# Optimization experiments

Measured on AMD Instinct MI355X. Metric: run time of the kernel, lower is better.

## Reference

```python
import jax, jax.numpy as jnp
import numpy as np

NQ = 4  # circuit is hard-wired to a 4-qubit ring
INV_SQRT2 = 1.0 / float(np.sqrt(2.0))


def _apply_1q(state, g, w):
    # state: [E,2,2,2,2]; g: [2,2] (shared) or [E,2,2] (per-edge)
    state = jnp.moveaxis(state, 1 + w, -1)
    sub = 'eab,e...b->e...a' if g.ndim == 3 else 'ab,e...b->e...a'
    state = jnp.einsum(sub, g, state)
    return jnp.moveaxis(state, -1, 1 + w)


def _apply_cry(state, theta, c, t):
    # controlled-RY(theta) with control wire c, target wire t; theta: [E]
    st = jnp.moveaxis(state, (1 + c, 1 + t), (-2, -1))  # [..., c, t]
    co = jnp.cos(theta / 2)[:, None, None]
    si = jnp.sin(theta / 2)[:, None, None]
    a = st[..., 1, 0]
    b = st[..., 1, 1]
    n0 = co * a - si * b
    n1 = si * a + co * b
    st = jnp.stack([jnp.stack([st[..., 0, 0], st[..., 0, 1]], axis=-1),
                    jnp.stack([n0, n1], axis=-1)], axis=-2)
    return jnp.moveaxis(st, (-2, -1), (1 + c, 1 + t))


def _simulate(q, k, params):
    # q, k: [E, NQ] rotation angles; params: [NQ, 3]
    E = q.shape[0]
    state = jnp.zeros((E, 2 ** NQ), jnp.complex64).at[:, 0].set(1.0)
    state = state.reshape((E,) + (2,) * NQ)
    # RY(query[i]) on wire i
    for w in range(NQ):
        c = jnp.cos(q[:, w] / 2)
        s = jnp.sin(q[:, w] / 2)
        g = jnp.stack([jnp.stack([c, -s], -1), jnp.stack([s, c], -1)], -2)
        state = _apply_1q(state, g.astype(jnp.complex64), w)
    # Hadamard on all wires
    H = jnp.array([[1, 1], [1, -1]], jnp.complex64) * INV_SQRT2
    for w in range(NQ):
        state = _apply_1q(state, H, w)
    # CRY(key[i]) on (i, (i+1)%NQ)
    for w in range(NQ):
        state = _apply_cry(state, k[:, w], w, (w + 1) % NQ)
    # Rot(phi, theta, omega) = RZ(omega) RY(theta) RZ(phi) on each wire
    for w in range(NQ):
        phi, th, om = params[w, 0], params[w, 1], params[w, 2]
        ct = jnp.cos(th / 2)
        st_ = jnp.sin(th / 2)
        g = jnp.stack([
            jnp.stack([jnp.exp(-1j * (phi + om) / 2) * ct, -jnp.exp(1j * (phi - om) / 2) * st_]),
            jnp.stack([jnp.exp(-1j * (phi - om) / 2) * st_, jnp.exp(1j * (phi + om) / 2) * ct]),
        ]).astype(jnp.complex64)
        state = _apply_1q(state, g, w)
    # <Z_i> expectation values
    p = jnp.abs(state) ** 2  # [E,2,2,2,2] float32
    exps = []
    for i in range(NQ):
        axes = tuple(a for a in range(1, 1 + NQ) if a != 1 + i)
        m = p.sum(axes)  # [E, 2]
        exps.append(m[:, 0] - m[:, 1])
    return jnp.stack(exps, -1).mean(-1)  # [E]


def setup_inputs() -> dict:
    key = jax.random.key(0)
    ks = jax.random.split(key, 7)
    N, D, E = 50000, 256, 800000
    node_features = jax.random.normal(ks[0], (N, D), jnp.float32)
    edge_index = jax.random.randint(ks[1], (2, E), 0, N)
    Wq = jax.random.normal(ks[2], (NQ, D), jnp.float32) / np.float32(np.sqrt(D))
    bq = jnp.zeros((NQ,), jnp.float32)
    Wk = jax.random.normal(ks[3], (NQ, D), jnp.float32) / np.float32(np.sqrt(D))
    bk = jnp.zeros((NQ,), jnp.float32)
    quantum_params = jax.random.normal(ks[4], (NQ, 3), jnp.float32) * 0.1
    return {'node_features': node_features, 'edge_index': edge_index,
            'Wq': Wq, 'bq': bq, 'Wk': Wk, 'bk': bk,
            'quantum_params': quantum_params}


def reference(node_features, edge_index, Wq, bq, Wk, bk, quantum_params):
    half_pi = np.float32(np.pi / 2)
    queries = jnp.tanh(node_features @ Wq.T + bq) * half_pi  # [N, NQ]
    keys = jnp.tanh(node_features @ Wk.T + bk) * half_pi     # [N, NQ]
    qe = queries[edge_index[0]]  # [E, NQ]
    ke = keys[edge_index[1]]     # [E, NQ]
    attn = _simulate(qe, ke, quantum_params)  # [E]
    return jax.nn.softmax(attn, axis=0)
```

## Files before the change

### kernel.cpp

```cpp
#include <hip/hip_runtime.h>
#include <math.h>

#define HALF_PI   1.57079632679489662f
#define INV_SQRT2 0.70710678118654752f
#define NPART     1024

__global__ __launch_bounds__(256) void node_qk(
        const float* __restrict__ feat,
        const float* __restrict__ Wq, const float* __restrict__ bq,
        const float* __restrict__ Wk, const float* __restrict__ bk,
        float* __restrict__ qtab, float* __restrict__ ktab, int N) {
    const int lane  = threadIdx.x & 63;
    const int wid   = (int)((blockIdx.x * blockDim.x + threadIdx.x) >> 6);
    const int nwid  = (int)((gridDim.x * blockDim.x) >> 6);

    float4 wq4[4], wk4[4];
    #pragma unroll
    for (int q = 0; q < 4; ++q) {
        wq4[q] = reinterpret_cast<const float4*>(Wq + q * 256)[lane];
        wk4[q] = reinterpret_cast<const float4*>(Wk + q * 256)[lane];
    }
    const int  g    = lane >> 3;
    const float bias = (g < 4) ? bq[g] : bk[g & 3];
    const bool hi  = (lane & 32) != 0;
    const bool s16 = (lane & 16) != 0;
    const bool s8  = (lane & 8)  != 0;

    for (int nb = wid * 2; nb < N; nb += nwid * 2) {
        const int  n1ok = (nb + 1 < N);
        float4 f0 = reinterpret_cast<const float4*>(feat)[(size_t)nb * 64 + lane];
        float4 f1 = n1ok ? reinterpret_cast<const float4*>(feat)[(size_t)(nb + 1) * 64 + lane]
                         : make_float4(0.f, 0.f, 0.f, 0.f);

        float acc0[8], acc1[8];
        #pragma unroll
        for (int q = 0; q < 4; ++q) {
            acc0[q]     = f0.x * wq4[q].x + f0.y * wq4[q].y + f0.z * wq4[q].z + f0.w * wq4[q].w;
            acc0[4 + q] = f0.x * wk4[q].x + f0.y * wk4[q].y + f0.z * wk4[q].z + f0.w * wk4[q].w;
            acc1[q]     = f1.x * wq4[q].x + f1.y * wq4[q].y + f1.z * wq4[q].z + f1.w * wq4[q].w;
            acc1[4 + q] = f1.x * wk4[q].x + f1.y * wk4[q].y + f1.z * wk4[q].z + f1.w * wk4[q].w;
        }

        #pragma unroll
        for (int p = 0; p < 2; ++p) {
            float* acc = (p == 0) ? acc0 : acc1;
            #pragma unroll
            for (int j = 0; j < 4; ++j) {
                float give = hi ? acc[j] : acc[j + 4];
                float r = __shfl_xor(give, 32, 64);
                acc[j]     += hi ? 0.f : r;
                acc[j + 4] += hi ? r : 0.f;
            }
            #pragma unroll
            for (int j = 0; j < 2; ++j) {
                float giveLow  = hi ? acc[6 + j] : acc[2 + j];
                float giveHigh = hi ? acc[4 + j] : acc[j];
                float give = s16 ? giveHigh : giveLow;
                float r = __shfl_xor(give, 16, 64);
                acc[j]     += (!hi && !s16) ? r : 0.f;
                acc[2 + j] += (!hi &&  s16) ? r : 0.f;
                acc[4 + j] += ( hi && !s16) ? r : 0.f;
                acc[6 + j] += ( hi &&  s16) ? r : 0.f;
            }
            float a_even = hi ? (s16 ? acc[6] : acc[4]) : (s16 ? acc[2] : acc[0]);
            float a_odd  = hi ? (s16 ? acc[7] : acc[5]) : (s16 ? acc[3] : acc[1]);
            float give3 = s8 ? a_even : a_odd;
            float r3 = __shfl_xor(give3, 8, 64);
            float v = (s8 ? a_odd : a_even) + r3;
            v += __shfl_xor(v, 4, 64);
            v += __shfl_xor(v, 2, 64);
            v += __shfl_xor(v, 1, 64);

            const int n = nb + p;
            if ((p == 0 || n1ok) && (lane & 7) == 0) {
                float t = tanhf(v + bias) * HALF_PI;
                if (g < 4) qtab[(size_t)n * 4 + g] = t;
                else       ktab[(size_t)n * 4 + (g & 3)] = t;
            }
        }
    }
}

__device__ __forceinline__ float edge_ex(float4 qv, float4 kv,
                                         const float* scz, const float* scx) {
    float qa[4] = {qv.x, qv.y, qv.z, qv.w};
    float ka[4] = {kv.x, kv.y, kv.z, kv.w};
    float u[4][2];
    #pragma unroll
    for (int w = 0; w < 4; ++w) {
        float s, c;
        __sincosf(qa[w] * 0.5f, &s, &c);
        u[w][0] = (c + s) * INV_SQRT2;
        u[w][1] = (c - s) * INV_SQRT2;
    }
    float a[16];
    #pragma unroll
    for (int x = 0; x < 16; ++x)
        a[x] = u[0][(x >> 3) & 1] * u[1][(x >> 2) & 1] *
               u[2][(x >> 1) & 1] * u[3][x & 1];
    #pragma unroll
    for (int w = 0; w < 4; ++w) {
        float si, co;
        __sincosf(ka[w] * 0.5f, &si, &co);
        const int cb = 1 << (3 - w);
        const int tb = 1 << (3 - ((w + 1) & 3));
        #pragma unroll
        for (int x = 0; x < 16; ++x) {
            if ((x & cb) && !(x & tb)) {
                float a0 = a[x], a1 = a[x | tb];
                a[x]      = co * a0 - si * a1;
                a[x | tb] = si * a0 + co * a1;
            }
        }
    }
    float attn = 0.f;
    #pragma unroll
    for (int q = 0; q < 4; ++q) {
        const int bit = 1 << (3 - q);
        float sz = 0.f, sx = 0.f;
        #pragma unroll
        for (int x = 0; x < 16; ++x) {
            float pp = a[x] * a[x];
            sz += (x & bit) ? -pp : pp;
            if (!(x & bit)) sx += a[x] * a[x | bit];
        }
        attn += scz[q] * sz - scx[q] * (2.f * sx);
    }
    return __expf(attn * 0.25f);
}

__global__ __launch_bounds__(256) void edge_attn(
        const int* __restrict__ ei,
        const float4* __restrict__ qtab, const float4* __restrict__ ktab,
        const float* __restrict__ qp,
        float* __restrict__ out, float* __restrict__ partial, int E) {
    __shared__ float scz[4], scx[4];
    __shared__ float red[256];
    const int tid = threadIdx.x;
    if (tid < 4) {
        float phi = qp[3 * tid + 0];
        float th  = qp[3 * tid + 1];
        float sth, cth;
        sincosf(th, &sth, &cth);
        scz[tid] = cth;
        scx[tid] = sth * cosf(phi);
    }
    __syncthreads();

    const int gtid  = blockIdx.x * 256 + tid;
    const int total = NPART * 256;

    int sidx[4], didx[4];
    #pragma unroll
    for (int it = 0; it < 4; ++it) {
        const int e  = gtid + it * total;
        const int ee = (e < E) ? e : (E - 1);
        sidx[it] = ei[ee];
        didx[it] = ei[E + ee];
    }

    float lsum = 0.f;
    #pragma unroll
    for (int it = 0; it < 4; ++it) {
        const int e = gtid + it * total;
        if (e < E) {
            float v = edge_ex(qtab[sidx[it]], ktab[didx[it]], scz, scx);
            out[e] = v;
            lsum += v;
        }
    }

    red[tid] = lsum;
    __syncthreads();
    #pragma unroll
    for (int s = 128; s > 0; s >>= 1) {
        if (tid < s) red[tid] += red[tid + s];
        __syncthreads();
    }
    if (tid == 0) partial[blockIdx.x] = red[0];
}

__global__ __launch_bounds__(256) void normalize_out(
        float* __restrict__ out, const float* __restrict__ partial, int E) {
    __shared__ float red[256];
    const int tid = threadIdx.x;
    float s = 0.f;
    #pragma unroll
    for (int k = 0; k < NPART / 256; ++k) s += partial[tid + k * 256];
    red[tid] = s;
    __syncthreads();
    #pragma unroll
    for (int st = 128; st > 0; st >>= 1) {
        if (tid < st) red[tid] += red[tid + st];
        __syncthreads();
    }
    const float inv = 1.f / red[0];

    const int nv4    = E >> 2;
    const int stride = (int)(gridDim.x * 256);
    float4* out4 = reinterpret_cast<float4*>(out);
    for (int i = blockIdx.x * 256 + tid; i < nv4; i += stride) {
        float4 v = out4[i];
        v.x *= inv; v.y *= inv; v.z *= inv; v.w *= inv;
        out4[i] = v;
    }
    const int tail = nv4 << 2;
    for (int e = tail + blockIdx.x * 256 + tid; e < E; e += stride)
        out[e] *= inv;
}

extern "C" void kernel_launch(void* const* d_in, const int* in_sizes, int n_in,
                              void* d_out, int out_size, void* d_ws, size_t ws_size,
                              hipStream_t stream) {
    const float* feat = (const float*)d_in[0];
    const int*   ei   = (const int*)d_in[1];
    const float* Wq   = (const float*)d_in[2];
    const float* bq   = (const float*)d_in[3];
    const float* Wk   = (const float*)d_in[4];
    const float* bk   = (const float*)d_in[5];
    const float* qp   = (const float*)d_in[6];

    int D = in_sizes[2] / 4;
    int N = in_sizes[0] / D;
    int E = in_sizes[1] / 2;
    (void)D;

    float* ws      = (float*)d_ws;
    float* partial = ws;
    float* qtab    = ws + NPART;
    float* ktab    = qtab + (size_t)N * 4;
    float* out     = (float*)d_out;

    node_qk<<<2048, 256, 0, stream>>>(feat, Wq, bq, Wk, bk, qtab, ktab, N);
    edge_attn<<<NPART, 256, 0, stream>>>(ei, (const float4*)qtab, (const float4*)ktab,
                                         qp, out, partial, E);
    normalize_out<<<1024, 256, 0, stream>>>(out, partial, E);
}
```

Measured before the change: 34.15 us.

## Store unnormalized exponentials as fp16 and fold Z-expectation weights algebraically

Edge exponentials are now written to a half-precision workspace buffer, and the normalize pass reads those halves and writes the fp32 output. Previously it read and wrote fp32 in place. This cuts intermediate memory traffic. The Z expectation terms are folded into 8 precomputed weights applied to symmetric probability differences, with the 0.25 and -2 scale factors moved into the constants, and the amplitude product is factored into two pairwise products. Storing in fp16 adds rounding error of about 1e-3 relative to each exponential, which may matter for tolerance checks.

Measured after the change: 32.84 us. 3.9% less time.

```diff
diff --git a/kernel.cpp b/kernel.cpp
--- a/kernel.cpp
+++ b/kernel.cpp
@@ -1,4 +1,5 @@
 #include <hip/hip_runtime.h>
+#include <hip/hip_fp16.h>
 #include <math.h>
 
 #define HALF_PI   1.57079632679489662f
@@ -82,59 +83,68 @@
 }
 
 __device__ __forceinline__ float edge_ex(float4 qv, float4 kv,
-                                         const float* scz, const float* scx) {
-    float qa[4] = {qv.x, qv.y, qv.z, qv.w};
-    float ka[4] = {kv.x, kv.y, kv.z, kv.w};
+                                         const float* W, const float* cx) {
     float u[4][2];
-    #pragma unroll
-    for (int w = 0; w < 4; ++w) {
-        float s, c;
-        __sincosf(qa[w] * 0.5f, &s, &c);
-        u[w][0] = (c + s) * INV_SQRT2;
-        u[w][1] = (c - s) * INV_SQRT2;
-    }
+    {
+        float qa[4] = {qv.x, qv.y, qv.z, qv.w};
+        #pragma unroll
+        for (int w = 0; w < 4; ++w) {
+            float s, c;
+            __sincosf(qa[w] * 0.5f, &s, &c);
+            u[w][0] = (c + s) * INV_SQRT2;
+            u[w][1] = (c - s) * INV_SQRT2;
+        }
+    }
+    float c01[4] = {u[0][0]*u[1][0], u[0][0]*u[1][1], u[0][1]*u[1][0], u[0][1]*u[1][1]};
+    float c23[4] = {u[2][0]*u[3][0], u[2][0]*u[3][1], u[2][1]*u[3][0], u[2][1]*u[3][1]};
     float a[16];
     #pragma unroll
-    for (int x = 0; x < 16; ++x)
-        a[x] = u[0][(x >> 3) & 1] * u[1][(x >> 2) & 1] *
-               u[2][(x >> 1) & 1] * u[3][x & 1];
-    #pragma unroll
-    for (int w = 0; w < 4; ++w) {
-        float si, co;
-        __sincosf(ka[w] * 0.5f, &si, &co);
-        const int cb = 1 << (3 - w);
-        const int tb = 1 << (3 - ((w + 1) & 3));
-        #pragma unroll
-        for (int x = 0; x < 16; ++x) {
-            if ((x & cb) && !(x & tb)) {
-                float a0 = a[x], a1 = a[x | tb];
-                a[x]      = co * a0 - si * a1;
-                a[x | tb] = si * a0 + co * a1;
-            }
-        }
-    }
+    for (int x = 0; x < 16; ++x) a[x] = c01[x >> 2] * c23[x & 3];
+
+    {
+        float ka[4] = {kv.x, kv.y, kv.z, kv.w};
+        #pragma unroll
+        for (int w = 0; w < 4; ++w) {
+            float si, co;
+            __sincosf(ka[w] * 0.5f, &si, &co);
+            const int cb = 1 << (3 - w);
+            const int tb = 1 << (3 - ((w + 1) & 3));
+            #pragma unroll
+            for (int x = 0; x < 16; ++x) {
+                if ((x & cb) && !(x & tb)) {
+                    float a0 = a[x], a1 = a[x | tb];
+                    a[x]      = co * a0 - si * a1;
+                    a[x | tb] = si * a0 + co * a1;
+                }
+            }
+        }
+    }
+
     float attn = 0.f;
+    #pragma unroll
+    for (int x = 0; x < 8; ++x) {
+        float pu = a[15 - x] * a[15 - x];
+        float d  = __builtin_fmaf(a[x], a[x], -pu);
+        attn = __builtin_fmaf(W[x], d, attn);
+    }
     #pragma unroll
     for (int q = 0; q < 4; ++q) {
         const int bit = 1 << (3 - q);
-        float sz = 0.f, sx = 0.f;
-        #pragma unroll
-        for (int x = 0; x < 16; ++x) {
-            float pp = a[x] * a[x];
-            sz += (x & bit) ? -pp : pp;
-            if (!(x & bit)) sx += a[x] * a[x | bit];
-        }
-        attn += scz[q] * sz - scx[q] * (2.f * sx);
-    }
-    return __expf(attn * 0.25f);
+        float sx = 0.f;
+        #pragma unroll
+        for (int x = 0; x < 16; ++x)
+            if (!(x & bit)) sx = __builtin_fmaf(a[x], a[x | bit], sx);
+        attn = __builtin_fmaf(cx[q], sx, attn);
+    }
+    return __expf(attn);
 }
 
 __global__ __launch_bounds__(256) void edge_attn(
         const int* __restrict__ ei,
         const float4* __restrict__ qtab, const float4* __restrict__ ktab,
         const float* __restrict__ qp,
-        float* __restrict__ out, float* __restrict__ partial, int E) {
-    __shared__ float scz[4], scx[4];
+        __half* __restrict__ exh, float* __restrict__ partial, int E) {
+    __shared__ float scz[4], scxs[4];
     __shared__ float red[256];
     const int tid = threadIdx.x;
     if (tid < 4) {
@@ -142,10 +152,17 @@
         float th  = qp[3 * tid + 1];
         float sth, cth;
         sincosf(th, &sth, &cth);
-        scz[tid] = cth;
-        scx[tid] = sth * cosf(phi);
+        scz[tid]  = 0.25f * cth;
+        scxs[tid] = -0.5f * sth * cosf(phi);
     }
     __syncthreads();
+
+    const float z0 = scz[0], z1 = scz[1], z2 = scz[2], z3 = scz[3];
+    const float u0 = z2 + z3, u1 = z2 - z3;
+    const float w00 = z1 + u0, w01 = z1 + u1, w10 = z1 - u1, w11 = z1 - u0;
+    const float W[8] = {z0 + w00, z0 + w01, z0 + w10, z0 + w11,
+                        z0 - w11, z0 - w10, z0 - w01, z0 - w00};
+    const float cx[4] = {scxs[0], scxs[1], scxs[2], scxs[3]};
 
     const int gtid  = blockIdx.x * 256 + tid;
     const int total = NPART * 256;
@@ -164,9 +181,10 @@
     for (int it = 0; it < 4; ++it) {
         const int e = gtid + it * total;
         if (e < E) {
-            float v = edge_ex(qtab[sidx[it]], ktab[didx[it]], scz, scx);
-            out[e] = v;
-            lsum += v;
+            float v = edge_ex(qtab[sidx[it]], ktab[didx[it]], W, cx);
+            __half h = __float2half(v);
+            exh[e] = h;
+            lsum += __half2float(h);
         }
     }
 
@@ -181,7 +199,8 @@
 }
 
 __global__ __launch_bounds__(256) void normalize_out(
-        float* __restrict__ out, const float* __restrict__ partial, int E) {
+        const __half* __restrict__ exh, const float* __restrict__ partial,
+        float* __restrict__ out, int E) {
     __shared__ float red[256];
     const int tid = threadIdx.x;
     float s = 0.f;
@@ -196,17 +215,26 @@
     }
     const float inv = 1.f / red[0];
 
-    const int nv4    = E >> 2;
+    const int nv8    = E >> 3;
     const int stride = (int)(gridDim.x * 256);
+    const uint4* exh8 = reinterpret_cast<const uint4*>(exh);
     float4* out4 = reinterpret_cast<float4*>(out);
-    for (int i = blockIdx.x * 256 + tid; i < nv4; i += stride) {
-        float4 v = out4[i];
-        v.x *= inv; v.y *= inv; v.z *= inv; v.w *= inv;
-        out4[i] = v;
-    }
-    const int tail = nv4 << 2;
+    for (int i = blockIdx.x * 256 + tid; i < nv8; i += stride) {
+        uint4 hv = exh8[i];
+        __half2 h0 = *reinterpret_cast<__half2*>(&hv.x);
+        __half2 h1 = *reinterpret_cast<__half2*>(&hv.y);
+        __half2 h2 = *reinterpret_cast<__half2*>(&hv.z);
+        __half2 h3 = *reinterpret_cast<__half2*>(&hv.w);
+        float2 f0 = __half22float2(h0);
+        float2 f1 = __half22float2(h1);
+        float2 f2 = __half22float2(h2);
+        float2 f3 = __half22float2(h3);
+        out4[2 * i]     = make_float4(f0.x * inv, f0.y * inv, f1.x * inv, f1.y * inv);
+        out4[2 * i + 1] = make_float4(f2.x * inv, f2.y * inv, f3.x * inv, f3.y * inv);
+    }
+    const int tail = nv8 << 3;
     for (int e = tail + blockIdx.x * 256 + tid; e < E; e += stride)
-        out[e] *= inv;
+        out[e] = __half2float(exh[e]) * inv;
 }
 
 extern "C" void kernel_launch(void* const* d_in, const int* in_sizes, int n_in,
@@ -225,14 +253,15 @@
     int E = in_sizes[1] / 2;
     (void)D;
 
-    float* ws      = (float*)d_ws;
-    float* partial = ws;
-    float* qtab    = ws + NPART;
-    float* ktab    = qtab + (size_t)N * 4;
-    float* out     = (float*)d_out;
+    float*  ws      = (float*)d_ws;
+    float*  partial = ws;
+    float*  qtab    = ws + NPART;
+    float*  ktab    = qtab + (size_t)N * 4;
+    __half* exh     = (__half*)(ktab + (size_t)N * 4);
+    float*  out     = (float*)d_out;
 
     node_qk<<<2048, 256, 0, stream>>>(feat, Wq, bq, Wk, bk, qtab, ktab, N);
     edge_attn<<<NPART, 256, 0, stream>>>(ei, (const float4*)qtab, (const float4*)ktab,
-                                         qp, out, partial, E);
-    normalize_out<<<1024, 256, 0, stream>>>(out, partial, E);
-}
+                                         qp, exh, partial, E);
+    normalize_out<<<1024, 256, 0, stream>>>(exh, partial, out, E);
+}
```
